# Performance work log

Hardware: AMD Instinct MI355X
Metric: run time of the kernel (lower is better)

## Reference

```python
import math
import jax, jax.numpy as jnp
import numpy as np

B, S, D, QK, H = 4, 4096, 1024, 128, 2048  # hidden = int(2.0 * dim)
NUM_BUCKETS, MAX_DIST = 32, 128
LN_EPS = 1e-5


def setup_inputs() -> dict:
    key = jax.random.key(0)
    ks = jax.random.split(key, 7)
    x = jax.random.normal(ks[0], (B, S, D), jnp.float32)
    ln_g = jnp.ones((D,), jnp.float32)
    ln_b = jnp.zeros((D,), jnp.float32)
    Wh = jax.random.normal(ks[1], (D, 2 * H), jnp.float32) * 0.02
    bh = jnp.zeros((2 * H,), jnp.float32)
    Wqk = jax.random.normal(ks[2], (D, QK), jnp.float32) * 0.02
    bqk = jnp.zeros((QK,), jnp.float32)
    os_gamma = jax.random.normal(ks[3], (2, QK), jnp.float32) * 0.02  # nn.init.normal_(std=0.02)
    os_beta = jnp.zeros((2, QK), jnp.float32)
    Wo = jax.random.normal(ks[4], (H, D), jnp.float32) * 0.02
    bo = jnp.zeros((D,), jnp.float32)
    rel_emb = jax.random.normal(ks[5], (NUM_BUCKETS, 1), jnp.float32) * 0.02
    return {"x": x, "ln_g": ln_g, "ln_b": ln_b, "Wh": Wh, "bh": bh,
            "Wqk": Wqk, "bqk": bqk, "os_gamma": os_gamma, "os_beta": os_beta,
            "Wo": Wo, "bo": bo, "rel_emb": rel_emb}


def _t5_rel_bias(rel_emb, seq_len, scale):
    # non-causal T5 relative position bucket (num_buckets halved to 16)
    pos = jnp.arange(seq_len)
    rel = pos[None, :] - pos[:, None]  # k_pos - q_pos -> [i, j]
    n = -rel
    nb = NUM_BUCKETS // 2  # 16
    me = nb // 2           # max_exact = 8
    ret = (n < 0).astype(jnp.int32) * nb
    na = jnp.abs(n)
    val_large = me + (jnp.log(jnp.maximum(na, 1).astype(jnp.float32) / me)
                      / math.log(MAX_DIST / me) * (nb - me)).astype(jnp.int32)
    val_large = jnp.minimum(val_large, nb - 1)
    bucket = ret + jnp.where(na < me, na, val_large)  # [S, S] in [0, 31]
    return rel_emb[bucket, 0] * scale  # [S, S]


def reference(x, ln_g, ln_b, Wh, bh, Wqk, bqk, os_gamma, os_beta, Wo, bo, rel_emb):
    seq_len = x.shape[-2]
    # LayerNorm
    mu = jnp.mean(x, axis=-1, keepdims=True)
    var = jnp.mean(jnp.square(x - mu), axis=-1, keepdims=True)
    normed = (x - mu) * jax.lax.rsqrt(var + LN_EPS) * ln_g + ln_b
    # hidden (v, gate) with SiLU
    hidden = jax.nn.silu(normed @ Wh + bh)  # [B, S, 2H]
    v, gate = hidden[..., :H], hidden[..., H:]
    # qk projection + offset/scale into q, k
    qk = jax.nn.silu(normed @ Wqk + bqk)  # [B, S, QK]
    q = qk * os_gamma[0] + os_beta[0]
    k = qk * os_gamma[1] + os_beta[1]
    sim = jnp.einsum('bid,bjd->bij', q, k)  # [B, S, S]
    sim = sim + _t5_rel_bias(rel_emb, seq_len, float(D) ** 0.5)
    attn = jnp.square(jax.nn.relu(sim / seq_len))  # ReLU^2, no softmax
    out = jnp.einsum('bij,bjd->bid', attn, v) * gate  # [B, S, H]
    out = out @ Wo + bo
    return out + x  # add_residual
```

## Files before the change

kernel.cpp:

```cpp
#include <hip/hip_runtime.h>
#include <hip/hip_bf16.h>
#include <math.h>

typedef __bf16 bf16_t;
typedef __bf16 bf16x8 __attribute__((ext_vector_type(8)));
typedef __bf16 bf16x4 __attribute__((ext_vector_type(4)));
typedef float  f32x4  __attribute__((ext_vector_type(4)));
typedef int    i32x4  __attribute__((ext_vector_type(4)));

#define S_LEN 4096
#define D_DIM 1024
#define QK_DIM 128
#define H_DIM 2048
#define BATCH 4

__device__ __forceinline__ void gld_lds16(const void* g, void* l) {
  __builtin_amdgcn_global_load_lds((const __attribute__((address_space(1))) void*)g,
                                   (__attribute__((address_space(3))) void*)l, 16, 0, 0);
}

__device__ __forceinline__ float silu_f(float v) {
  return v / (1.0f + __expf(-v));
}

__device__ __forceinline__ bf16x8 as_bf(i32x4 v) {
  union { i32x4 a; bf16x8 b; } u; u.a = v; return u.b;
}

__device__ __forceinline__ float ldf(const void* p, size_t i, int f32) {
  return f32 ? ((const float*)p)[i] : (float)((const bf16_t*)p)[i];
}

__global__ void probe_k(const unsigned* __restrict__ ln_g_raw, int* __restrict__ flag) {
  if (threadIdx.x == 0) flag[0] = (ln_g_raw[0] == 0x3F800000u) ? 1 : 0;
}

#define M_HID 0
#define M_QK 1
#define M_SCORE 2
#define M_PV 3
#define M_OUT 4

template <int MODE, int K, int BM>
__global__ __launch_bounds__(512, (BM == 256 ? 2 : 4))
void gemm3(const bf16_t* __restrict__ A, const bf16_t* __restrict__ Bt,
           const void* e0, const void* e1, const float* __restrict__ ef,
           void* o0, void* o1, const int* __restrict__ dflag)
{
  constexpr int MR  = BM / 32;
  constexpr int ASLOT = BM * 64;
  constexpr int BSLOT = 16384;
  constexpr int NT  = K / 32;
  constexpr int RA  = BM / 128;
  constexpr int SLD = RA + 2;

  __shared__ __align__(16) char lds[3 * (ASLOT + BSLOT)];

  const int t = threadIdx.x;
  const int w = t >> 6, lane = t & 63;
  const int quad = lane >> 4, col = lane & 15;
  const int wm = (w >> 2) * (BM / 2);
  const int wn = (w & 3) * 64;

  const int gx = gridDim.x;
  const int nwg = gx * (int)gridDim.y;
  const int orig = (int)blockIdx.y * gx + (int)blockIdx.x;
  const int wg = (orig & 7) * (nwg >> 3) + (orig >> 3);
  const int bx = wg & (gx - 1), by = wg >> __builtin_ctz(gx);
  const int m0 = bx * BM, n0 = by * 256;

  const bf16_t* const Ap = A + (size_t)m0 * K;
  const bf16_t* const Bp = Bt + (size_t)n0 * K;

  size_t aoff[RA], boff[2];
#pragma unroll
  for (int c = 0; c < RA; ++c) {
    const int P = c * 8192 + t * 16;
    const int L = P ^ (((P >> 7) & 3) << 4);
    aoff[c] = (size_t)(L >> 6) * K + ((L & 63) >> 1);
  }
#pragma unroll
  for (int c = 0; c < 2; ++c) {
    const int P = c * 8192 + t * 16;
    const int L = P ^ (((P >> 7) & 3) << 4);
    boff[c] = (size_t)(L >> 6) * K + ((L & 63) >> 1);
  }

  const int xr = (quad ^ ((col >> 1) & 3)) << 4;
  const unsigned ldsI = (unsigned)(size_t)&lds[0];
  const unsigned aStat = ldsI + (unsigned)((wm + col) * 64 + xr);
  const unsigned bStat = ldsI + 3u * ASLOT + (unsigned)((wn + col) * 64 + xr);

  f32x4 acc[MR][4] = {};
  i32x4 aF[MR], bF[4];

#define SB() __builtin_amdgcn_sched_barrier(0)
#define BARR() do { SB(); __builtin_amdgcn_s_barrier(); SB(); } while (0)
#define DSR(dst, addr, lit) \
  asm volatile("ds_read_b128 %0, %1 offset:" #lit : "=v"(dst) : "v"(addr))
#define WAITL0() asm volatile("s_waitcnt lgkmcnt(0)" ::: "memory")
#define WAITV0() asm volatile("s_waitcnt vmcnt(0)" ::: "memory")
#define VWS() do {                                                             \
    if constexpr (SLD == 3) asm volatile("s_waitcnt vmcnt(3)" ::: "memory");   \
    else                    asm volatile("s_waitcnt vmcnt(4)" ::: "memory");   \
  } while (0)

#define RD() do {                                                              \
    const unsigned aAd = aStat + (unsigned)(bsel * ASLOT);                     \
    const unsigned bAd = bStat + (unsigned)(bsel * BSLOT);                     \
    DSR(aF[0], aAd, 0);    DSR(aF[1], aAd, 1024);                              \
    DSR(aF[2], aAd, 2048); DSR(aF[3], aAd, 3072);                              \
    if constexpr (MR == 8) {                                                   \
      DSR(aF[4], aAd, 4096); DSR(aF[5], aAd, 5120);                            \
      DSR(aF[6], aAd, 6144); DSR(aF[7], aAd, 7168);                            \
    }                                                                          \
    DSR(bF[0], bAd, 0);    DSR(bF[1], bAd, 1024);                              \
    DSR(bF[2], bAd, 2048); DSR(bF[3], bAd, 3072);                              \
  } while (0)

#define MM() do {                                                              \
    __builtin_amdgcn_s_setprio(1);                                             \
    _Pragma("unroll") for (int mi = 0; mi < MR; ++mi)                          \
    _Pragma("unroll") for (int ni = 0; ni < 4; ++ni)                           \
      acc[mi][ni] = __builtin_amdgcn_mfma_f32_16x16x32_bf16(                   \
          as_bf(aF[mi]), as_bf(bF[ni]), acc[mi][ni], 0, 0, 0);                 \
    __builtin_amdgcn_s_setprio(0);                                             \
  } while (0)

#define STG(ts, sl) do {                                                       \
    char* da_ = (char*)lds + (sl) * ASLOT + t * 16;                            \
    char* db_ = (char*)lds + 3 * ASLOT + (sl) * BSLOT + t * 16;                \
    const bf16_t* ga_ = Ap + (size_t)(ts) * 32;                                \
    const bf16_t* gb_ = Bp + (size_t)(ts) * 32;                                \
    _Pragma("unroll") for (int c_ = 0; c_ < RA; ++c_)                          \
      gld_lds16(ga_ + aoff[c_], da_ + c_ * 8192);                              \
    _Pragma("unroll") for (int c_ = 0; c_ < 2; ++c_)                           \
      gld_lds16(gb_ + boff[c_], db_ + c_ * 8192);                              \
  } while (0)

  STG(0, 0);
  STG(1, 1);
  VWS();
  BARR();

  int bsel = 0, ssel = 2;
  for (int tt = 0; tt < NT; ++tt) {
    RD();
    if (tt + 2 < NT) STG(tt + 2, ssel);
    WAITL0(); SB();
    MM();
    SB();
    if (tt + 1 < NT) {
      if (tt + 2 < NT) VWS();
      else WAITV0();
    }
    BARR();
    bsel = (bsel == 2) ? 0 : bsel + 1;
    ssel = (ssel == 2) ? 0 : ssel + 1;
  }

#undef SB
#undef BARR
#undef DSR
#undef WAITL0
#undef WAITV0
#undef VWS
#undef RD
#undef MM
#undef STG

  __syncthreads();

  int f32 = 0;
  if constexpr (MODE == M_HID || MODE == M_OUT) f32 = dflag[0];

  if constexpr (MODE == M_OUT) {
    float (*swzf)[16][68] = (float (*)[16][68])lds;
#pragma unroll
    for (int m = 0; m < MR; ++m) {
      __syncthreads();
#pragma unroll
      for (int j = 0; j < 4; ++j)
#pragma unroll
        for (int r = 0; r < 4; ++r)
          swzf[w][quad * 4 + r][j * 16 + col] = acc[m][j][r];
      __syncthreads();
#pragma unroll
      for (int it = 0; it < 4; ++it) {
        const int task = it * 64 + lane, gr = task >> 4, ch = task & 15;
        const int gm = m0 + wm + m * 16 + gr;
        const int gnc = n0 + wn + ch * 4;
        f32x4 vv = *(const f32x4*)&swzf[w][gr][ch * 4];
        float xr4[4], r4[4];
        if (f32) {
          float4 t4 = *(const float4*)((const float*)e1 + (size_t)gm * D_DIM + gnc);
          xr4[0] = t4.x; xr4[1] = t4.y; xr4[2] = t4.z; xr4[3] = t4.w;
        } else {
          bf16x4 t4 = *(const bf16x4*)((const bf16_t*)e1 + (size_t)gm * D_DIM + gnc);
#pragma unroll
          for (int qq = 0; qq < 4; ++qq) xr4[qq] = (float)t4[qq];
        }
#pragma unroll
        for (int qq = 0; qq < 4; ++qq)
          r4[qq] = vv[qq] + ldf(e0, gnc + qq, f32) + xr4[qq];
        if (f32) {
          float4 s4 = {r4[0], r4[1], r4[2], r4[3]};
          *(float4*)((float*)o0 + (size_t)gm * D_DIM + gnc) = s4;
        } else {
          bf16x4 s4;
#pragma unroll
          for (int qq = 0; qq < 4; ++qq) s4[qq] = (bf16_t)r4[qq];
          *(bf16x4*)((bf16_t*)o0 + (size_t)gm * D_DIM + gnc) = s4;
        }
      }
    }
    return;
  }

  if constexpr (MODE == M_HID) {
    if (n0 < H_DIM) {
      constexpr int TW = MR * 16 + 8;
      bf16_t (*swzT)[16][TW] = (bf16_t (*)[16][TW])lds;
      const int bb  = m0 >> 12;
      const int smb = (m0 + wm) & (S_LEN - 1);
#pragma unroll
      for (int j = 0; j < 4; ++j) {
        __syncthreads();
        const int gnj = n0 + wn + j * 16;
        const float bhv = ldf(e0, gnj + col, f32);
#pragma unroll
        for (int m = 0; m < MR; ++m)
#pragma unroll
          for (int r = 0; r < 4; ++r)
            swzT[w][col][m * 16 + quad * 4 + r] = (bf16_t)silu_f(acc[m][j][r] + bhv);
        __syncthreads();
#pragma unroll
        for (int it = 0; it < MR / 2; ++it) {
          const int task = it * 64 + lane;
          const int gr = task / (MR * 2), ch = task & (MR * 2 - 1);
          bf16x8 vv = *(const bf16x8*)&swzT[w][gr][ch * 8];
          const size_t off = ((size_t)bb * H_DIM + (gnj + gr)) * S_LEN + smb + ch * 8;
          *(bf16x8*)((bf16_t*)o0 + off) = vv;
        }
      }
      return;
    }
  }

  if constexpr (MODE == M_HID || MODE == M_SCORE || MODE == M_PV) {
    bf16_t (*swzb)[16][72] = (bf16_t (*)[16][72])lds;
#pragma unroll
    for (int m = 0; m < MR; ++m) {
      __syncthreads();
#pragma unroll
      for (int j = 0; j < 4; ++j) {
        const int gn = n0 + wn + j * 16 + col;
#pragma unroll
        for (int r = 0; r < 4; ++r) {
          const float val = acc[m][j][r];
          bf16_t sv;
          if constexpr (MODE == M_HID) {
            sv = (bf16_t)silu_f(val + ldf(e0, gn, f32));
          } else if constexpr (MODE == M_SCORE) {
            const int gm = m0 + wm + m * 16 + quad * 4 + r;
            float wgt = fmaxf((val + ef[gm - gn + (S_LEN - 1)]) *
                              (1.0f / (float)S_LEN), 0.0f);
            sv = (bf16_t)(wgt * wgt);
          } else {
            sv = (bf16_t)val;
          }
          swzb[w][quad * 4 + r][j * 16 + col] = sv;
        }
      }
      __syncthreads();
#pragma unroll
      for (int it = 0; it < 2; ++it) {
        const int task = it * 64 + lane, gr = task >> 3, ch = task & 7;
        const int gm  = m0 + wm + m * 16 + gr;
        const int gnb = n0 + wn + ch * 8;
        bf16x8 vv = *(const bf16x8*)&swzb[w][gr][ch * 8];
        if constexpr (MODE == M_HID) {
          *(bf16x8*)((bf16_t*)o1 + (size_t)gm * H_DIM + (gnb - H_DIM)) = vv;
        } else if constexpr (MODE == M_SCORE) {
          *(bf16x8*)((bf16_t*)o0 + (size_t)gm * S_LEN + gnb) = vv;
        } else {
          bf16x8 g8 = *(const bf16x8*)((const bf16_t*)e0 + (size_t)gm * H_DIM + gnb);
          bf16x8 r8;
#pragma unroll
          for (int qq = 0; qq < 8; ++qq)
            r8[qq] = (bf16_t)((float)vv[qq] * (float)g8[qq]);
          *(bf16x8*)((bf16_t*)o0 + (size_t)gm * H_DIM + gnb) = r8;
        }
      }
    }
  }
}

template <int MODE>
__global__ __launch_bounds__(256)
void gemm_bt(const bf16_t* __restrict__ A, const bf16_t* __restrict__ Bt,
             int M, int N, int K,
             const void* e0, const void* e1, const void* e2,
             const float* __restrict__ ef,
             void* o0, void* o1, const int* __restrict__ dflag)
{
  __shared__ __align__(16) bf16_t As[128 * 32];
  __shared__ __align__(16) bf16_t Bs[128 * 32];
  const int t = threadIdx.x;
  const int w = t >> 6, lane = t & 63;
  const int quad = lane >> 4, col = lane & 15;
  const int wm = (w >> 1) << 6, wn = (w & 1) << 6;
  const int m0 = blockIdx.x * 128, n0 = blockIdx.y * 128;
  const int f32 = dflag[0];

  f32x4 acc[4][4] = {};

  for (int k0 = 0; k0 < K; k0 += 32) {
    __syncthreads();
    for (int p = 0; p < 2; ++p) {
      const int chunk = w * 2 + p;
      const int fl = (chunk * 64 + lane) * 8;
      const int r = fl >> 5, c = fl & 31;
      gld_lds16(A  + (size_t)(m0 + r) * K + (k0 + c), &As[chunk * 512]);
      gld_lds16(Bt + (size_t)(n0 + r) * K + (k0 + c), &Bs[chunk * 512]);
    }
    __syncthreads();

    bf16x8 af[4], bfr[4];
#pragma unroll
    for (int i = 0; i < 4; ++i)
      af[i] = *(const bf16x8*)&As[(wm + i * 16 + col) * 32 + quad * 8];
#pragma unroll
    for (int i = 0; i < 4; ++i)
      bfr[i] = *(const bf16x8*)&Bs[(wn + i * 16 + col) * 32 + quad * 8];
#pragma unroll
    for (int i = 0; i < 4; ++i)
#pragma unroll
      for (int j = 0; j < 4; ++j)
        acc[i][j] = __builtin_amdgcn_mfma_f32_16x16x32_bf16(af[i], bfr[j], acc[i][j], 0, 0, 0);
  }

#pragma unroll
  for (int i = 0; i < 4; ++i) {
#pragma unroll
    for (int j = 0; j < 4; ++j) {
#pragma unroll
      for (int r = 0; r < 4; ++r) {
        const int gm = m0 + wm + i * 16 + quad * 4 + r;
        const int gn = n0 + wn + j * 16 + col;
        float val = acc[i][j][r] + ldf(e0, gn, f32);
        float s = silu_f(val);
        ((bf16_t*)o0)[(size_t)gm * QK_DIM + gn] =
            (bf16_t)(s * ldf(e1, gn, f32) + ldf(e2, gn, f32));
        ((bf16_t*)o1)[(size_t)gm * QK_DIM + gn] =
            (bf16_t)(s * ldf(e1, QK_DIM + gn, f32) + ldf(e2, QK_DIM + gn, f32));
      }
    }
  }
}

__global__ __launch_bounds__(256)
void layernorm_k(const void* __restrict__ x, const void* __restrict__ g,
                 const void* __restrict__ be, bf16_t* __restrict__ out,
                 const int* __restrict__ dflag)
{
  const int row = blockIdx.x;
  const int t = threadIdx.x;
  const int f32 = dflag[0];
  float f[4];
  if (f32) {
    const float* xr = (const float*)x + (size_t)row * D_DIM;
    float4 xv = *(const float4*)&xr[t * 4];
    f[0] = xv.x; f[1] = xv.y; f[2] = xv.z; f[3] = xv.w;
  } else {
    const bf16_t* xr = (const bf16_t*)x + (size_t)row * D_DIM;
    bf16x4 xv = *(const bf16x4*)&xr[t * 4];
#pragma unroll
    for (int i = 0; i < 4; ++i) f[i] = (float)xv[i];
  }
  float s = 0.f, sq = 0.f;
#pragma unroll
  for (int i = 0; i < 4; ++i) { s += f[i]; sq += f[i] * f[i]; }
#pragma unroll
  for (int off = 32; off > 0; off >>= 1) {
    s += __shfl_down(s, off);
    sq += __shfl_down(sq, off);
  }
  __shared__ float red[8];
  const int w = t >> 6;
  if ((t & 63) == 0) { red[w] = s; red[4 + w] = sq; }
  __syncthreads();
  s = red[0] + red[1] + red[2] + red[3];
  sq = red[4] + red[5] + red[6] + red[7];
  const float mu = s * (1.0f / D_DIM);
  const float var = sq * (1.0f / D_DIM) - mu * mu;
  const float inv = rsqrtf(var + 1e-5f);
  bf16x4 ov;
#pragma unroll
  for (int i = 0; i < 4; ++i) {
    float nv = (f[i] - mu) * inv * ldf(g, t * 4 + i, f32) + ldf(be, t * 4 + i, f32);
    ov[i] = (bf16_t)nv;
  }
  *(bf16x4*)&out[(size_t)row * D_DIM + t * 4] = ov;
}

__global__ __launch_bounds__(256)
void transpose_k(const void* __restrict__ src, bf16_t* __restrict__ dst,
                 int R, int C, const int* __restrict__ dflag)
{
  __shared__ bf16_t tile[32][33];
  const int f32 = dflag[0];
  const int c0 = blockIdx.x * 32, r0 = blockIdx.y * 32;
  for (int i = threadIdx.y; i < 32; i += 8)
    tile[i][threadIdx.x] = (bf16_t)ldf(src, (size_t)(r0 + i) * C + (c0 + threadIdx.x), f32);
  __syncthreads();
  for (int i = threadIdx.y; i < 32; i += 8)
    dst[(size_t)(c0 + i) * R + (r0 + threadIdx.x)] = tile[threadIdx.x][i];
}

__global__ void bias_k(const void* __restrict__ rel_emb, float* __restrict__ bias,
                       const int* __restrict__ dflag)
{
  int d = blockIdx.x * 256 + threadIdx.x;
  if (d >= 2 * S_LEN - 1) return;
  const int f32 = dflag[0];
  int n = d - (S_LEN - 1);
  int ret = (n < 0) ? 16 : 0;
  int na = n < 0 ? -n : n;
  int b;
  if (na < 8) b = na;
  else {
    float vl = logf((float)na * (1.0f / 8.0f)) / logf(16.0f) * 8.0f;
    int vi = 8 + (int)vl;
    b = vi > 15 ? 15 : vi;
  }
  bias[d] = ldf(rel_emb, ret + b, f32) * 32.0f;
}

extern "C" void kernel_launch(void* const* d_in, const int* in_sizes, int n_in,
                              void* d_out, int out_size, void* d_ws, size_t ws_size,
                              hipStream_t stream)
{
  const void* x    = d_in[0];
  const void* ln_g = d_in[1];
  const void* ln_b = d_in[2];
  const void* Wh   = d_in[3];
  const void* bh   = d_in[4];
  const void* Wqk  = d_in[5];
  const void* bqk  = d_in[6];
  const void* osg  = d_in[7];
  const void* osb  = d_in[8];
  const void* Wo   = d_in[9];
  const void* bo   = d_in[10];
  const void* rel  = d_in[11];

  const int BS = BATCH * S_LEN;
  char* p = (char*)d_ws;
  int*    flags  = (int*)p;     p += 256;
  float*  bias   = (float*)p;   p += (size_t)8192 * 4;
  bf16_t* WhT    = (bf16_t*)p;  p += (size_t)4096 * 1024 * 2;
  bf16_t* WqkT   = (bf16_t*)p;  p += (size_t)128 * 1024 * 2;
  bf16_t* WoT    = (bf16_t*)p;  p += (size_t)1024 * 2048 * 2;
  bf16_t* q      = (bf16_t*)p;  p += (size_t)BS * QK_DIM * 2;
  bf16_t* kk     = (bf16_t*)p;  p += (size_t)BS * QK_DIM * 2;
  bf16_t* vT     = (bf16_t*)p;  p += (size_t)BS * H_DIM * 2;
  bf16_t* gate   = (bf16_t*)p;  p += (size_t)BS * H_DIM * 2;
  bf16_t* normed = (bf16_t*)p;  p += (size_t)BS * D_DIM * 2;
  bf16_t* attn   = normed;
  bf16_t* pvg    = gate;

  probe_k<<<1, 64, 0, stream>>>((const unsigned*)ln_g, flags);
  bias_k<<<32, 256, 0, stream>>>(rel, bias, flags);
  transpose_k<<<dim3(4096 / 32, 1024 / 32), dim3(32, 8), 0, stream>>>(Wh, WhT, 1024, 4096, flags);
  transpose_k<<<dim3(128 / 32, 1024 / 32), dim3(32, 8), 0, stream>>>(Wqk, WqkT, 1024, 128, flags);
  transpose_k<<<dim3(1024 / 32, 2048 / 32), dim3(32, 8), 0, stream>>>(Wo, WoT, 2048, 1024, flags);
  layernorm_k<<<BS, 256, 0, stream>>>(x, ln_g, ln_b, normed, flags);

  gemm3<M_HID, 1024, 256><<<dim3(BS / 256, 4096 / 256), 512, 0, stream>>>(
      normed, WhT, bh, nullptr, nullptr, vT, gate, flags);
  gemm_bt<M_QK><<<dim3(BS / 128, 1), 256, 0, stream>>>(
      normed, WqkT, BS, QK_DIM, 1024, bqk, osg, osb, nullptr, q, kk, flags);

  for (int b = 0; b < BATCH; ++b) {
    gemm3<M_SCORE, QK_DIM, 128><<<dim3(S_LEN / 128, S_LEN / 256), 512, 0, stream>>>(
        q + (size_t)b * S_LEN * QK_DIM, kk + (size_t)b * S_LEN * QK_DIM,
        nullptr, nullptr, bias, attn, nullptr, flags);
    gemm3<M_PV, S_LEN, 128><<<dim3(S_LEN / 128, H_DIM / 256), 512, 0, stream>>>(
        attn, vT + (size_t)b * S_LEN * H_DIM,
        gate + (size_t)b * S_LEN * H_DIM, nullptr, nullptr,
        pvg + (size_t)b * S_LEN * H_DIM, nullptr, flags);
  }

  gemm3<M_OUT, H_DIM, 256><<<dim3(BS / 256, 1024 / 256), 512, 0, stream>>>(
      pvg, WoT, bo, x, nullptr, d_out, nullptr, flags);
}
```

Baseline: 818.2 us.

## Generalize GEMM to K-step 64 with fine-grained LDS waits, fixed 128-row tiles

Replaces the BM-templated GEMM with one templated on the K-step per stage (32 or 64), fixing M tiles at 128 rows. The PV GEMM now stages 64-wide K slices with an 8-way XOR swizzle, halving the number of barriers per K. Inside each stage, MFMAs start as soon as their LDS fragments arrive via stepped lgkmcnt waits instead of one full wait. HID and OUT GEMMs move from 256-row to 128-row tiles, which doubles the workgroup count but lowers per-block operand reuse.

```diff
diff --git a/kernel.cpp b/kernel.cpp
--- a/kernel.cpp
+++ b/kernel.cpp
@@ -41,25 +41,28 @@
 #define M_PV 3
 #define M_OUT 4
 
-template <int MODE, int K, int BM>
-__global__ __launch_bounds__(512, (BM == 256 ? 2 : 4))
-void gemm3(const bf16_t* __restrict__ A, const bf16_t* __restrict__ Bt,
+template <int MODE, int K, int KS>
+__global__ __launch_bounds__(512, (KS == 64 ? 2 : 4))
+void gemm4(const bf16_t* __restrict__ A, const bf16_t* __restrict__ Bt,
            const void* e0, const void* e1, const float* __restrict__ ef,
            void* o0, void* o1, const int* __restrict__ dflag)
 {
-  constexpr int MR  = BM / 32;
-  constexpr int ASLOT = BM * 64;
-  constexpr int BSLOT = 16384;
-  constexpr int NT  = K / 32;
-  constexpr int RA  = BM / 128;
-  constexpr int SLD = RA + 2;
+  constexpr int NT   = K / KS;
+  constexpr int NSL  = KS / 32;
+  constexpr int ASLOT = 128 * KS * 2;
+  constexpr int BSLOT = 256 * KS * 2;
+  constexpr int RA   = ASLOT / 8192;
+  constexpr int RB   = BSLOT / 8192;
+  constexpr int SLD  = RA + RB;
+  constexpr int MR   = 4;
+  constexpr int RWB  = KS * 2;
 
   __shared__ __align__(16) char lds[3 * (ASLOT + BSLOT)];
 
   const int t = threadIdx.x;
   const int w = t >> 6, lane = t & 63;
   const int quad = lane >> 4, col = lane & 15;
-  const int wm = (w >> 2) * (BM / 2);
+  const int wm = (w >> 2) * 64;
   const int wn = (w & 3) * 64;
 
   const int gx = gridDim.x;
@@ -67,74 +70,59 @@
   const int orig = (int)blockIdx.y * gx + (int)blockIdx.x;
   const int wg = (orig & 7) * (nwg >> 3) + (orig >> 3);
   const int bx = wg & (gx - 1), by = wg >> __builtin_ctz(gx);
-  const int m0 = bx * BM, n0 = by * 256;
+  const int m0 = bx * 128, n0 = by * 256;
 
   const bf16_t* const Ap = A + (size_t)m0 * K;
   const bf16_t* const Bp = Bt + (size_t)n0 * K;
 
-  size_t aoff[RA], boff[2];
+  size_t aoff[RA], boff[RB];
 #pragma unroll
   for (int c = 0; c < RA; ++c) {
     const int P = c * 8192 + t * 16;
-    const int L = P ^ (((P >> 7) & 3) << 4);
-    aoff[c] = (size_t)(L >> 6) * K + ((L & 63) >> 1);
-  }
-#pragma unroll
-  for (int c = 0; c < 2; ++c) {
+    const int L = P ^ (((P >> 7) & (NSL == 1 ? 3 : 7)) << 4);
+    aoff[c] = (size_t)(L / RWB) * K + ((L & (RWB - 1)) >> 1);
+  }
+#pragma unroll
+  for (int c = 0; c < RB; ++c) {
     const int P = c * 8192 + t * 16;
-    const int L = P ^ (((P >> 7) & 3) << 4);
-    boff[c] = (size_t)(L >> 6) * K + ((L & 63) >> 1);
-  }
-
-  const int xr = (quad ^ ((col >> 1) & 3)) << 4;
+    const int L = P ^ (((P >> 7) & (NSL == 1 ? 3 : 7)) << 4);
+    boff[c] = (size_t)(L / RWB) * K + ((L & (RWB - 1)) >> 1);
+  }
+
+  const int xr = (NSL == 1) ? ((quad ^ ((col >> 1) & 3)) << 4)
+                            : ((quad ^ (col & 7)) << 4);
   const unsigned ldsI = (unsigned)(size_t)&lds[0];
-  const unsigned aStat = ldsI + (unsigned)((wm + col) * 64 + xr);
-  const unsigned bStat = ldsI + 3u * ASLOT + (unsigned)((wn + col) * 64 + xr);
+  const unsigned aStat = ldsI + (unsigned)((wm + col) * RWB + xr);
+  const unsigned bStat = ldsI + 3u * ASLOT + (unsigned)((wn + col) * RWB + xr);
 
   f32x4 acc[MR][4] = {};
-  i32x4 aF[MR], bF[4];
+  i32x4 aF[MR][NSL], bF[4][NSL];
 
 #define SB() __builtin_amdgcn_sched_barrier(0)
 #define BARR() do { SB(); __builtin_amdgcn_s_barrier(); SB(); } while (0)
 #define DSR(dst, addr, lit) \
   asm volatile("ds_read_b128 %0, %1 offset:" #lit : "=v"(dst) : "v"(addr))
-#define WAITL0() asm volatile("s_waitcnt lgkmcnt(0)" ::: "memory")
+#define WL(n) asm volatile("s_waitcnt lgkmcnt(" #n ")" ::: "memory")
 #define WAITV0() asm volatile("s_waitcnt vmcnt(0)" ::: "memory")
 #define VWS() do {                                                             \
     if constexpr (SLD == 3) asm volatile("s_waitcnt vmcnt(3)" ::: "memory");   \
-    else                    asm volatile("s_waitcnt vmcnt(4)" ::: "memory");   \
+    else                    asm volatile("s_waitcnt vmcnt(6)" ::: "memory");   \
   } while (0)
 
-#define RD() do {                                                              \
-    const unsigned aAd = aStat + (unsigned)(bsel * ASLOT);                     \
-    const unsigned bAd = bStat + (unsigned)(bsel * BSLOT);                     \
-    DSR(aF[0], aAd, 0);    DSR(aF[1], aAd, 1024);                              \
-    DSR(aF[2], aAd, 2048); DSR(aF[3], aAd, 3072);                              \
-    if constexpr (MR == 8) {                                                   \
-      DSR(aF[4], aAd, 4096); DSR(aF[5], aAd, 5120);                            \
-      DSR(aF[6], aAd, 6144); DSR(aF[7], aAd, 7168);                            \
-    }                                                                          \
-    DSR(bF[0], bAd, 0);    DSR(bF[1], bAd, 1024);                              \
-    DSR(bF[2], bAd, 2048); DSR(bF[3], bAd, 3072);                              \
-  } while (0)
-
-#define MM() do {                                                              \
-    __builtin_amdgcn_s_setprio(1);                                             \
-    _Pragma("unroll") for (int mi = 0; mi < MR; ++mi)                          \
-    _Pragma("unroll") for (int ni = 0; ni < 4; ++ni)                           \
-      acc[mi][ni] = __builtin_amdgcn_mfma_f32_16x16x32_bf16(                   \
-          as_bf(aF[mi]), as_bf(bF[ni]), acc[mi][ni], 0, 0, 0);                 \
-    __builtin_amdgcn_s_setprio(0);                                             \
-  } while (0)
+#define MMI(mi, ni, kk)                                                        \
+  acc[mi][ni] = __builtin_amdgcn_mfma_f32_16x16x32_bf16(                       \
+      as_bf(aF[mi][kk]), as_bf(bF[ni][kk]), acc[mi][ni], 0, 0, 0)
+#define MM4(ni, kk) do { MMI(0, ni, kk); MMI(1, ni, kk);                       \
+                         MMI(2, ni, kk); MMI(3, ni, kk); } while (0)
 
 #define STG(ts, sl) do {                                                       \
     char* da_ = (char*)lds + (sl) * ASLOT + t * 16;                            \
     char* db_ = (char*)lds + 3 * ASLOT + (sl) * BSLOT + t * 16;                \
-    const bf16_t* ga_ = Ap + (size_t)(ts) * 32;                                \
-    const bf16_t* gb_ = Bp + (size_t)(ts) * 32;                                \
+    const bf16_t* ga_ = Ap + (size_t)(ts) * KS;                                \
+    const bf16_t* gb_ = Bp + (size_t)(ts) * KS;                                \
     _Pragma("unroll") for (int c_ = 0; c_ < RA; ++c_)                          \
       gld_lds16(ga_ + aoff[c_], da_ + c_ * 8192);                              \
-    _Pragma("unroll") for (int c_ = 0; c_ < 2; ++c_)                           \
+    _Pragma("unroll") for (int c_ = 0; c_ < RB; ++c_)                          \
       gld_lds16(gb_ + boff[c_], db_ + c_ * 8192);                              \
   } while (0)
 
@@ -145,10 +133,63 @@
 
   int bsel = 0, ssel = 2;
   for (int tt = 0; tt < NT; ++tt) {
-    RD();
-    if (tt + 2 < NT) STG(tt + 2, ssel);
-    WAITL0(); SB();
-    MM();
+    const unsigned aAd = aStat + (unsigned)(bsel * ASLOT);
+    const unsigned bAd = bStat + (unsigned)(bsel * BSLOT);
+    if constexpr (NSL == 1) {
+      DSR(bF[0][0], bAd, 0);
+      DSR(aF[0][0], aAd, 0);
+      DSR(aF[1][0], aAd, 1024);
+      DSR(aF[2][0], aAd, 2048);
+      DSR(aF[3][0], aAd, 3072);
+      DSR(bF[1][0], bAd, 1024);
+      DSR(bF[2][0], bAd, 2048);
+      DSR(bF[3][0], bAd, 3072);
+      if (tt + 2 < NT) STG(tt + 2, ssel);
+      __builtin_amdgcn_s_setprio(1);
+      WL(6); SB(); MMI(0, 0, 0);
+      WL(5); SB(); MMI(1, 0, 0);
+      WL(4); SB(); MMI(2, 0, 0);
+      WL(3); SB(); MMI(3, 0, 0);
+      WL(2); SB(); MM4(1, 0);
+      WL(1); SB(); MM4(2, 0);
+      WL(0); SB(); MM4(3, 0);
+      __builtin_amdgcn_s_setprio(0);
+    } else {
+      const unsigned aA1 = aAd ^ 64u, bA1 = bAd ^ 64u;
+      DSR(bF[0][0], bAd, 0);
+      DSR(aF[0][0], aAd, 0);
+      DSR(aF[1][0], aAd, 2048);
+      DSR(aF[2][0], aAd, 4096);
+      DSR(aF[3][0], aAd, 6144);
+      DSR(bF[1][0], bAd, 2048);
+      DSR(bF[2][0], bAd, 4096);
+      DSR(bF[3][0], bAd, 6144);
+      DSR(bF[0][1], bA1, 0);
+      DSR(aF[0][1], aA1, 0);
+      DSR(aF[1][1], aA1, 2048);
+      DSR(aF[2][1], aA1, 4096);
+      DSR(aF[3][1], aA1, 6144);
+      DSR(bF[1][1], bA1, 2048);
+      DSR(bF[2][1], bA1, 4096);
+      DSR(bF[3][1], bA1, 6144);
+      if (tt + 2 < NT) STG(tt + 2, ssel);
+      __builtin_amdgcn_s_setprio(1);
+      WL(14); SB(); MMI(0, 0, 0);
+      WL(13); SB(); MMI(1, 0, 0);
+      WL(12); SB(); MMI(2, 0, 0);
+      WL(11); SB(); MMI(3, 0, 0);
+      WL(10); SB(); MM4(1, 0);
+      WL(9);  SB(); MM4(2, 0);
+      WL(8);  SB(); MM4(3, 0);
+      WL(6);  SB(); MMI(0, 0, 1);
+      WL(5);  SB(); MMI(1, 0, 1);
+      WL(4);  SB(); MMI(2, 0, 1);
+      WL(3);  SB(); MMI(3, 0, 1);
+      WL(2);  SB(); MM4(1, 1);
+      WL(1);  SB(); MM4(2, 1);
+      WL(0);  SB(); MM4(3, 1);
+      __builtin_amdgcn_s_setprio(0);
+    }
     SB();
     if (tt + 1 < NT) {
       if (tt + 2 < NT) VWS();
@@ -162,11 +203,11 @@
 #undef SB
 #undef BARR
 #undef DSR
-#undef WAITL0
+#undef WL
 #undef WAITV0
 #undef VWS
-#undef RD
-#undef MM
+#undef MMI
+#undef MM4
 #undef STG
 
   __syncthreads();
@@ -219,8 +260,7 @@
 
   if constexpr (MODE == M_HID) {
     if (n0 < H_DIM) {
-      constexpr int TW = MR * 16 + 8;
-      bf16_t (*swzT)[16][TW] = (bf16_t (*)[16][TW])lds;
+      bf16_t (*swzT)[16][72] = (bf16_t (*)[16][72])lds;
       const int bb  = m0 >> 12;
       const int smb = (m0 + wm) & (S_LEN - 1);
 #pragma unroll
@@ -235,9 +275,8 @@
             swzT[w][col][m * 16 + quad * 4 + r] = (bf16_t)silu_f(acc[m][j][r] + bhv);
         __syncthreads();
 #pragma unroll
-        for (int it = 0; it < MR / 2; ++it) {
-          const int task = it * 64 + lane;
-          const int gr = task / (MR * 2), ch = task & (MR * 2 - 1);
+        for (int it = 0; it < 2; ++it) {
+          const int task = it * 64 + lane, gr = task >> 3, ch = task & 7;
           bf16x8 vv = *(const bf16x8*)&swzT[w][gr][ch * 8];
           const size_t off = ((size_t)bb * H_DIM + (gnj + gr)) * S_LEN + smb + ch * 8;
           *(bf16x8*)((bf16_t*)o0 + off) = vv;
@@ -476,21 +515,21 @@
   transpose_k<<<dim3(1024 / 32, 2048 / 32), dim3(32, 8), 0, stream>>>(Wo, WoT, 2048, 1024, flags);
   layernorm_k<<<BS, 256, 0, stream>>>(x, ln_g, ln_b, normed, flags);
 
-  gemm3<M_HID, 1024, 256><<<dim3(BS / 256, 4096 / 256), 512, 0, stream>>>(
+  gemm4<M_HID, 1024, 32><<<dim3(BS / 128, 4096 / 256), 512, 0, stream>>>(
       normed, WhT, bh, nullptr, nullptr, vT, gate, flags);
   gemm_bt<M_QK><<<dim3(BS / 128, 1), 256, 0, stream>>>(
       normed, WqkT, BS, QK_DIM, 1024, bqk, osg, osb, nullptr, q, kk, flags);
 
   for (int b = 0; b < BATCH; ++b) {
-    gemm3<M_SCORE, QK_DIM, 128><<<dim3(S_LEN / 128, S_LEN / 256), 512, 0, stream>>>(
+    gemm4<M_SCORE, QK_DIM, 32><<<dim3(S_LEN / 128, S_LEN / 256), 512, 0, stream>>>(
         q + (size_t)b * S_LEN * QK_DIM, kk + (size_t)b * S_LEN * QK_DIM,
         nullptr, nullptr, bias, attn, nullptr, flags);
-    gemm3<M_PV, S_LEN, 128><<<dim3(S_LEN / 128, H_DIM / 256), 512, 0, stream>>>(
+    gemm4<M_PV, S_LEN, 64><<<dim3(S_LEN / 128, H_DIM / 256), 512, 0, stream>>>(
         attn, vT + (size_t)b * S_LEN * H_DIM,
         gate + (size_t)b * S_LEN * H_DIM, nullptr, nullptr,
         pvg + (size_t)b * S_LEN * H_DIM, nullptr, flags);
   }
 
-  gemm3<M_OUT, H_DIM, 256><<<dim3(BS / 256, 1024 / 256), 512, 0, stream>>>(
+  gemm4<M_OUT, H_DIM, 32><<<dim3(BS / 128, 1024 / 256), 512, 0, stream>>>(
       pvg, WoT, bo, x, nullptr, d_out, nullptr, flags);
 }
```

Result: faster. 770.0 us (-5.9%).
